# Kernel optimization log

Measured on AMD Instinct MI355X. Metric: run time of the kernel, lower is better.

The kernel has to match this reference:

```python
import jax, jax.numpy as jnp
from jax import lax
import numpy as np
import math

EMBED_DIM = 1024
NUM_HEADS = 16
REDUCTION = 2


def setup_inputs() -> dict:
    key = jax.random.key(0)
    ks = jax.random.split(key, 11)
    B, N, C = 2, 4096, EMBED_DIM
    s = 1.0 / math.sqrt(C)
    return {
        "x": jax.random.normal(ks[0], (B, N, C), jnp.float32),
        "q_w": jax.random.normal(ks[1], (C, C), jnp.float32) * s,
        "q_b": jax.random.normal(ks[2], (C,), jnp.float32) * s,
        "k_w": jax.random.normal(ks[3], (C, C), jnp.float32) * s,
        "k_b": jax.random.normal(ks[4], (C,), jnp.float32) * s,
        "v_w": jax.random.normal(ks[5], (C, C), jnp.float32) * s,
        "v_b": jax.random.normal(ks[6], (C,), jnp.float32) * s,
        "conv_w": jax.random.normal(ks[7], (C, 1, 3), jnp.float32) * 0.5,
        "conv_b": jax.random.normal(ks[8], (C,), jnp.float32) * 0.1,
        "out_w": jax.random.normal(ks[9], (C, C), jnp.float32) * s,
        "out_b": jax.random.normal(ks[10], (C,), jnp.float32) * s,
    }


def reference(x, q_w, q_b, k_w, k_b, v_w, v_b, conv_w, conv_b, out_w, out_b):
    B, N, C = x.shape
    H = NUM_HEADS
    D = C // H
    scale = 1.0 / math.sqrt(D)

    q = x @ q_w.T + q_b  # [B,N,C]

    # depthwise conv1d KV downsample: kernel=3, stride=REDUCTION, pad=1, groups=C
    xd = jnp.transpose(x, (0, 2, 1))  # [B,C,N]
    xd = lax.conv_general_dilated(
        xd, conv_w, window_strides=(REDUCTION,), padding=[(1, 1)],
        feature_group_count=C, dimension_numbers=("NCH", "OIH", "NCH"))
    xd = xd + conv_b[None, :, None]
    xd = jnp.transpose(xd, (0, 2, 1))  # [B,Nk,C]

    k = xd @ k_w.T + k_b
    v = xd @ v_w.T + v_b

    Nk = k.shape[1]
    q = q.reshape(B, N, H, D).transpose(0, 2, 1, 3)   # [B,H,N,D]
    k = k.reshape(B, Nk, H, D).transpose(0, 2, 1, 3)  # [B,H,Nk,D]
    v = v.reshape(B, Nk, H, D).transpose(0, 2, 1, 3)

    att = jnp.einsum("bhnd,bhmd->bhnm", q, k) * scale  # [B,H,N,Nk]
    att = jax.nn.softmax(att, axis=-1)
    out = jnp.einsum("bhnm,bhmd->bhnd", att, v)        # [B,H,N,D]
    out = out.transpose(0, 2, 1, 3).reshape(B, N, C)
    return out @ out_w.T + out_b
```

## Files before the change

kernel.cpp:

```cpp
#include <hip/hip_runtime.h>
#include <stdint.h>
#include <stddef.h>


using bf16x8 = __attribute__((ext_vector_type(8))) short;
using f32x4  = __attribute__((ext_vector_type(4))) float;
using f32x16 = __attribute__((ext_vector_type(16))) float;
using u16x4  = __attribute__((ext_vector_type(4))) unsigned short;
using u32x4  = __attribute__((ext_vector_type(4))) uint32_t;

#if defined(__has_builtin)
#if __has_builtin(__builtin_amdgcn_exp2f)
#define FAST_EXP2(x) __builtin_amdgcn_exp2f(x)
#endif
#endif
#ifndef FAST_EXP2
extern "C" __device__ float __ocml_native_exp2_f32(float);
#define FAST_EXP2(x) __ocml_native_exp2_f32(x)
#endif

__device__ __forceinline__ unsigned short f2bf(float f) {
  union { float f; uint32_t u; } v; v.f = f;
  uint32_t r = v.u + 0x7fffu + ((v.u >> 16) & 1u);
  return (unsigned short)(r >> 16);
}

__device__ __forceinline__ uint32_t cvt_pk_bf16(float lo, float hi) {
  uint32_t r;
  asm("v_cvt_pk_bf16_f32 %0, %1, %2" : "=v"(r) : "v"(lo), "v"(hi));
  return r;
}

__device__ __forceinline__ void plane32_swap(uint32_t& a, uint32_t& b) {
  asm("v_permlane32_swap_b32 %0, %1" : "+v"(a), "+v"(b));
}

__global__ __launch_bounds__(256)
void cast_bf16_kernel(const float* __restrict__ in, unsigned short* __restrict__ out, int n) {
  int i = (blockIdx.x * 256 + threadIdx.x) * 8;
  if (i >= n) return;
  float4 a = *(const float4*)(in + i);
  float4 b = *(const float4*)(in + i + 4);
  u16x4 r0 = {f2bf(a.x), f2bf(a.y), f2bf(a.z), f2bf(a.w)};
  u16x4 r1 = {f2bf(b.x), f2bf(b.y), f2bf(b.z), f2bf(b.w)};
  *(u16x4*)(out + i) = r0;
  *(u16x4*)(out + i + 4) = r1;
}

struct WPtrs { const float* p0; const float* p1; const float* p2; const float* p3; };
__global__ __launch_bounds__(256)
void cast4_bf16_kernel(WPtrs in, unsigned short* __restrict__ out) {
  int which = blockIdx.x >> 9;
  int i = ((blockIdx.x & 511) * 256 + threadIdx.x) * 8;
  const float* src = (which == 0) ? in.p0 : (which == 1) ? in.p1
                   : (which == 2) ? in.p2 : in.p3;
  unsigned short* dst = out + (size_t)which * 1048576;
  float4 a = *(const float4*)(src + i);
  float4 b = *(const float4*)(src + i + 4);
  u16x4 r0 = {f2bf(a.x), f2bf(a.y), f2bf(a.z), f2bf(a.w)};
  u16x4 r1 = {f2bf(b.x), f2bf(b.y), f2bf(b.z), f2bf(b.w)};
  *(u16x4*)(dst + i) = r0;
  *(u16x4*)(dst + i + 4) = r1;
}

__global__ __launch_bounds__(256)
void conv_ds_kernel(const float* __restrict__ x, const float* __restrict__ cw,
                    const float* __restrict__ cb, unsigned short* __restrict__ xd) {
  int row = blockIdx.x;
  int b = row >> 11, m = row & 2047;
  int c = threadIdx.x * 4;
  const float* xb = x + (size_t)b * 4096 * 1024;
  int n0 = 2 * m - 1;
  float4 x0 = {0.f, 0.f, 0.f, 0.f};
  if (n0 >= 0) x0 = *(const float4*)(xb + (size_t)n0 * 1024 + c);
  float4 x1 = *(const float4*)(xb + (size_t)(2 * m) * 1024 + c);
  float4 x2 = *(const float4*)(xb + (size_t)(2 * m + 1) * 1024 + c);
  float4 w0 = *(const float4*)(cw + c * 3);
  float4 w1 = *(const float4*)(cw + c * 3 + 4);
  float4 w2 = *(const float4*)(cw + c * 3 + 8);
  float4 bb = *(const float4*)(cb + c);
  float r0 = x0.x * w0.x + x1.x * w0.y + x2.x * w0.z + bb.x;
  float r1 = x0.y * w0.w + x1.y * w1.x + x2.y * w1.y + bb.y;
  float r2 = x0.z * w1.z + x1.z * w1.w + x2.z * w2.x + bb.z;
  float r3 = x0.w * w2.y + x1.w * w2.z + x2.w * w2.w + bb.w;
  u16x4 r = {f2bf(r0), f2bf(r1), f2bf(r2), f2bf(r3)};
  *(u16x4*)(xd + (size_t)row * 1024 + c) = r;
}

template<int OUT_MODE>
__global__ __launch_bounds__(256)
void gemm_bt(const unsigned short* __restrict__ A, const unsigned short* __restrict__ W,
             const float* __restrict__ bias, const float* __restrict__ bias2,
             void* __restrict__ out, void* __restrict__ out2,
             int M, int N, int K) {
  __shared__ unsigned short As[128 * 32];
  __shared__ unsigned short Bs[128 * 32];
  const int tid = threadIdx.x;
  const int w = tid >> 6, lane = tid & 63;
  const int nbn = N >> 7;
  const int bm = blockIdx.x / nbn, bn = blockIdx.x % nbn;
  const int wr = w >> 1, wc = w & 1;
  const int l15 = lane & 15, l4 = lane >> 4;

  f32x4 acc[4][4];
#pragma unroll
  for (int m = 0; m < 4; ++m)
#pragma unroll
    for (int n = 0; n < 4; ++n) acc[m][n] = (f32x4)0.0f;

  const int arow = bm * 128 + w * 16 + (lane >> 2);
  const int brow = bn * 128 + w * 16 + (lane >> 2);
  const int kcol = (lane & 3) * 8;

  for (int kt = 0; kt < K; kt += 32) {
#pragma unroll
    for (int p = 0; p < 2; ++p) {
      __builtin_amdgcn_global_load_lds(
          (const __attribute__((address_space(1))) void*)(A + (size_t)(arow + p * 64) * K + kt + kcol),
          (__attribute__((address_space(3))) void*)(As + p * 2048 + w * 512), 16, 0, 0);
      __builtin_amdgcn_global_load_lds(
          (const __attribute__((address_space(1))) void*)(W + (size_t)(brow + p * 64) * K + kt + kcol),
          (__attribute__((address_space(3))) void*)(Bs + p * 2048 + w * 512), 16, 0, 0);
    }
    __syncthreads();
    bf16x8 af[4], bf[4];
#pragma unroll
    for (int m = 0; m < 4; ++m) af[m] = *(const bf16x8*)(As + (wr * 64 + m * 16 + l15) * 32 + l4 * 8);
#pragma unroll
    for (int n = 0; n < 4; ++n) bf[n] = *(const bf16x8*)(Bs + (wc * 64 + n * 16 + l15) * 32 + l4 * 8);
#pragma unroll
    for (int m = 0; m < 4; ++m)
#pragma unroll
      for (int n = 0; n < 4; ++n)
        acc[m][n] = __builtin_amdgcn_mfma_f32_16x16x32_bf16(af[m], bf[n], acc[m][n], 0, 0, 0);
    __syncthreads();
  }

  const bool vregion = (OUT_MODE == 3) && (bn >= 8);
#pragma unroll
  for (int n = 0; n < 4; ++n) {
    int col = bn * 128 + wc * 64 + n * 16 + l15;
    float bv = vregion ? bias2[col - 1024] : bias[col];
#pragma unroll
    for (int m = 0; m < 4; ++m) {
      int row0 = bm * 128 + wr * 64 + m * 16 + l4 * 4;
      if (vregion) {
        int b = row0 >> 11, kv = row0 & 2047;
        u16x4 r = {f2bf(acc[m][n][0] + bv), f2bf(acc[m][n][1] + bv),
                   f2bf(acc[m][n][2] + bv), f2bf(acc[m][n][3] + bv)};
        *(u16x4*)((unsigned short*)out2 + ((size_t)(b * 1024 + (col - 1024))) * 2048 + kv) = r;
      } else if (OUT_MODE == 1 || OUT_MODE == 3) {
        const int ldn = (OUT_MODE == 3) ? 1024 : N;
#pragma unroll
        for (int i = 0; i < 4; ++i)
          ((unsigned short*)out)[(size_t)(row0 + i) * ldn + col] = f2bf(acc[m][n][i] + bv);
      } else {
#pragma unroll
        for (int i = 0; i < 4; ++i)
          ((float*)out)[(size_t)(row0 + i) * N + col] = acc[m][n][i] + bv;
      }
    }
  }
}

#define ATT_SCL_L2E 0.18033688011112043f

__global__ __launch_bounds__(256)
void flash_attn_kernel(const unsigned short* __restrict__ q,
                       const unsigned short* __restrict__ k,
                       const unsigned short* __restrict__ vt,
                       unsigned short* __restrict__ o) {
  const int bid = blockIdx.x;
  const int lin = (bid & 7) * 128 + (bid >> 3);
  const int qb = lin & 31;
  const int hb = lin >> 5;
  const int h = hb & 15, b = hb >> 4;

  const int tid = threadIdx.x;
  const int w = tid >> 6, lane = tid & 63;
  const int l31 = lane & 31, hi = lane >> 5;

  __shared__ unsigned short Ks[2][64 * 64];
  __shared__ unsigned short Vs[2][64 * 64];

  const size_t C = 1024;
  const int qrow = b * 4096 + qb * 128 + w * 32 + l31;

  bf16x8 qf[4];
#pragma unroll
  for (int ks = 0; ks < 4; ++ks)
    qf[ks] = *(const bf16x8*)(q + (size_t)qrow * C + h * 64 + ks * 16 + hi * 8);

  f32x16 o0 = (f32x16)0.0f, o1 = (f32x16)0.0f;
  float lrun = 0.f;

  const int srow = (tid & 7) | ((tid >> 5) << 3);
  const int sc2  = (tid >> 3) & 3;
  const int sxor = (srow & 7);
  const unsigned short* kbase = k  + ((size_t)(b * 2048 + srow)) * C + h * 64;
  const unsigned short* vbase = vt + ((size_t)(b * 1024 + h * 64 + srow)) * 2048;

  const int r0 = l31, r1 = 32 + l31;
  const int x0c = (r0 & 7) * 8, x1c = (r1 & 7) * 8;

  auto exppack = [&](f32x16& s0, f32x16& s1, u32x4 (&pw)[4]) {
    float rs0 = 0.f, rs1 = 0.f;
#pragma unroll
    for (int i = 0; i < 16; ++i) {
      float p0 = FAST_EXP2(s0[i] * ATT_SCL_L2E);
      float p1 = FAST_EXP2(s1[i] * ATT_SCL_L2E);
      s0[i] = p0; s1[i] = p1;
      rs0 += p0; rs1 += p1;
    }
    lrun += rs0 + rs1;
#pragma unroll
    for (int hh = 0; hh < 2; ++hh) {
#pragma unroll
      for (int cp = 0; cp < 2; ++cp) {
#pragma unroll
        for (int e = 0; e < 2; ++e) {
          float xa0 = (hh == 0) ? s0[8 * cp + 2 * e]     : s1[8 * cp + 2 * e];
          float xa1 = (hh == 0) ? s0[8 * cp + 2 * e + 1] : s1[8 * cp + 2 * e + 1];
          float xb0 = (hh == 0) ? s0[8 * cp + 4 + 2 * e]     : s1[8 * cp + 4 + 2 * e];
          float xb1 = (hh == 0) ? s0[8 * cp + 4 + 2 * e + 1] : s1[8 * cp + 4 + 2 * e + 1];
          uint32_t wa = cvt_pk_bf16(xa0, xa1);
          uint32_t wb = cvt_pk_bf16(xb0, xb1);
          plane32_swap(wa, wb);
          pw[2 * hh + cp][e]     = wa;
          pw[2 * hh + cp][e + 2] = wb;
        }
      }
    }
  };

  bf16x8 krg[2], vrg[2], tmp[2];
#pragma unroll
  for (int j = 0; j < 2; ++j) tmp[j] = *(const bf16x8*)(kbase + (sc2 + 4 * j) * 8);
#pragma unroll
  for (int j = 0; j < 2; ++j)
    *(bf16x8*)(&Ks[0][srow * 64 + (((sc2 + 4 * j) ^ sxor) * 8)]) = tmp[j];
#pragma unroll
  for (int j = 0; j < 2; ++j) tmp[j] = *(const bf16x8*)(kbase + (size_t)64 * C + (sc2 + 4 * j) * 8);
#pragma unroll
  for (int j = 0; j < 2; ++j)
    *(bf16x8*)(&Ks[1][srow * 64 + (((sc2 + 4 * j) ^ sxor) * 8)]) = tmp[j];
#pragma unroll
  for (int j = 0; j < 2; ++j) tmp[j] = *(const bf16x8*)(vbase + (sc2 + 4 * j) * 8);
#pragma unroll
  for (int j = 0; j < 2; ++j)
    *(bf16x8*)(&Vs[0][srow * 64 + (((sc2 + 4 * j) ^ sxor) * 8)]) = tmp[j];
#pragma unroll
  for (int j = 0; j < 2; ++j) {
    krg[j] = *(const bf16x8*)(kbase + (size_t)128 * C + (sc2 + 4 * j) * 8);
    vrg[j] = *(const bf16x8*)(vbase + 64 + (sc2 + 4 * j) * 8);
  }
  __syncthreads();

  u32x4 pwA[4], pwB[4];
  {
    f32x16 s0 = (f32x16)0.0f, s1 = (f32x16)0.0f;
    __builtin_amdgcn_s_setprio(1);
#pragma unroll
    for (int ks = 0; ks < 4; ++ks) {
      int coff = ks * 16 + hi * 8;
      bf16x8 kf0 = *(const bf16x8*)(&Ks[0][r0 * 64 + (coff ^ x0c)]);
      bf16x8 kf1 = *(const bf16x8*)(&Ks[0][r1 * 64 + (coff ^ x1c)]);
      s0 = __builtin_amdgcn_mfma_f32_32x32x16_bf16(kf0, qf[ks], s0, 0, 0, 0);
      s1 = __builtin_amdgcn_mfma_f32_32x32x16_bf16(kf1, qf[ks], s1, 0, 0, 0);
    }
    __builtin_amdgcn_s_setprio(0);
    exppack(s0, s1, pwA);
  }
  __syncthreads();

  auto body = [&](int t, u32x4 (&pwC)[4], u32x4 (&pwN)[4]) {
    const unsigned short* Vc = Vs[t & 1];
    f32x16 s0 = (f32x16)0.0f, s1 = (f32x16)0.0f;

    __builtin_amdgcn_s_setprio(1);
    if (t < 31) {
      const unsigned short* Kn = Ks[(t + 1) & 1];
#pragma unroll
      for (int ks = 0; ks < 4; ++ks) {
        int coff = ks * 16 + hi * 8;
        bf16x8 kf0 = *(const bf16x8*)(Kn + r0 * 64 + (coff ^ x0c));
        bf16x8 kf1 = *(const bf16x8*)(Kn + r1 * 64 + (coff ^ x1c));
        s0 = __builtin_amdgcn_mfma_f32_32x32x16_bf16(kf0, qf[ks], s0, 0, 0, 0);
        s1 = __builtin_amdgcn_mfma_f32_32x32x16_bf16(kf1, qf[ks], s1, 0, 0, 0);
      }
    }
#pragma unroll
    for (int ksv = 0; ksv < 4; ++ksv) {
      bf16x8 pv = __builtin_bit_cast(bf16x8, pwC[ksv]);
      int coff = ksv * 16 + hi * 8;
      bf16x8 vf0 = *(const bf16x8*)(Vc + r0 * 64 + (coff ^ x0c));
      bf16x8 vf1 = *(const bf16x8*)(Vc + r1 * 64 + (coff ^ x1c));
      o0 = __builtin_amdgcn_mfma_f32_32x32x16_bf16(vf0, pv, o0, 0, 0, 0);
      o1 = __builtin_amdgcn_mfma_f32_32x32x16_bf16(vf1, pv, o1, 0, 0, 0);
    }
    __builtin_amdgcn_s_setprio(0);

    if (t < 30) {
#pragma unroll
      for (int j = 0; j < 2; ++j)
        *(bf16x8*)(&((unsigned short*)Ks[t & 1])[srow * 64 + (((sc2 + 4 * j) ^ sxor) * 8)]) = krg[j];
    }
    if (t < 31) {
#pragma unroll
      for (int j = 0; j < 2; ++j)
        *(bf16x8*)(&((unsigned short*)Vs[(t + 1) & 1])[srow * 64 + (((sc2 + 4 * j) ^ sxor) * 8)]) = vrg[j];
    }
    if (t < 29) {
#pragma unroll
      for (int j = 0; j < 2; ++j)
        krg[j] = *(const bf16x8*)(kbase + (size_t)(t + 3) * 64 * C + (sc2 + 4 * j) * 8);
    }
    if (t < 30) {
#pragma unroll
      for (int j = 0; j < 2; ++j)
        vrg[j] = *(const bf16x8*)(vbase + (t + 2) * 64 + (sc2 + 4 * j) * 8);
    }

    if (t < 31) exppack(s0, s1, pwN);

    if (t < 31) __syncthreads();
  };

  for (int tt = 0; tt < 16; ++tt) {
    body(2 * tt,     pwA, pwB);
    body(2 * tt + 1, pwB, pwA);
  }

  float lsum = lrun + __shfl_xor(lrun, 32);
  const float inv = 1.0f / lsum;
  u32x4 ow[4];
#pragma unroll
  for (int c = 0; c < 4; ++c) {
#pragma unroll
    for (int e = 0; e < 2; ++e) {
      uint32_t wa = cvt_pk_bf16(o0[4 * c + 2 * e] * inv, o0[4 * c + 2 * e + 1] * inv);
      uint32_t wb = cvt_pk_bf16(o1[4 * c + 2 * e] * inv, o1[4 * c + 2 * e + 1] * inv);
      plane32_swap(wa, wb);
      ow[c][e]     = wa;
      ow[c][e + 2] = wb;
    }
  }
  unsigned short* op = o + (size_t)qrow * C + h * 64 + hi * 32;
#pragma unroll
  for (int ch = 0; ch < 4; ++ch)
    *(u32x4*)(op + ch * 8) = ow[ch];
}

extern "C" void kernel_launch(void* const* d_in, const int* in_sizes, int n_in,
                              void* d_out, int out_size, void* d_ws, size_t ws_size,
                              hipStream_t stream) {
  const float* x   = (const float*)d_in[0];
  const float* q_w = (const float*)d_in[1];
  const float* q_b = (const float*)d_in[2];
  const float* k_w = (const float*)d_in[3];
  const float* k_b = (const float*)d_in[4];
  const float* v_w = (const float*)d_in[5];
  const float* v_b = (const float*)d_in[6];
  const float* cw  = (const float*)d_in[7];
  const float* cb  = (const float*)d_in[8];
  const float* o_w = (const float*)d_in[9];
  const float* o_b = (const float*)d_in[10];
  float* out = (float*)d_out;

  unsigned short* ws    = (unsigned short*)d_ws;
  unsigned short* x_bf  = ws;
  unsigned short* qw_bf = x_bf + 8388608;
  unsigned short* kw_bf = qw_bf + 1048576;
  unsigned short* vw_bf = kw_bf + 1048576;
  unsigned short* ow_bf = vw_bf + 1048576;
  unsigned short* q_bf  = ow_bf + 1048576;
  unsigned short* xd_bf = q_bf + 8388608;
  unsigned short* k_bf  = xd_bf + 4194304;
  unsigned short* vt_bf = k_bf + 4194304;
  unsigned short* ao_bf = x_bf;

  cast_bf16_kernel<<<4096, 256, 0, stream>>>(x, x_bf, 8388608);
  WPtrs wp = {q_w, k_w, v_w, o_w};
  cast4_bf16_kernel<<<2048, 256, 0, stream>>>(wp, qw_bf);
  conv_ds_kernel<<<4096, 256, 0, stream>>>(x, cw, cb, xd_bf);

  gemm_bt<1><<<512, 256, 0, stream>>>(x_bf, qw_bf, q_b, nullptr, q_bf, nullptr,
                                      8192, 1024, 1024);
  gemm_bt<3><<<512, 256, 0, stream>>>(xd_bf, kw_bf, k_b, v_b, k_bf, vt_bf,
                                      4096, 2048, 1024);

  flash_attn_kernel<<<1024, 256, 0, stream>>>(q_bf, k_bf, vt_bf, ao_bf);

  gemm_bt<0><<<512, 256, 0, stream>>>(ao_bf, ow_bf, o_b, nullptr, out, nullptr,
                                      8192, 1024, 1024);
}
```

Measured before the change: 208.3 us.

## Fuse x cast into conv kernel, prescale Q, swizzle GEMM block order

Folds the fp32-to-bf16 cast of x into the depthwise conv kernel, which already loads rows 2m and 2m+1, so x is read from HBM only once and one launch goes away. The softmax scale times log2(e) is applied in the Q projection epilogue, which removes a multiply per score in the attention exp loop. GEMM block indices are also remapped in a stride-8 swizzle to change the tile scheduling order. Rounding Q to bf16 after scaling slightly changes its numerics.

```diff
diff --git a/kernel.cpp b/kernel.cpp
--- a/kernel.cpp
+++ b/kernel.cpp
@@ -8,6 +8,8 @@
 using f32x16 = __attribute__((ext_vector_type(16))) float;
 using u16x4  = __attribute__((ext_vector_type(4))) unsigned short;
 using u32x4  = __attribute__((ext_vector_type(4))) uint32_t;
+
+#define ATT_SCL_L2E 0.18033688011112043f
 
 #if defined(__has_builtin)
 #if __has_builtin(__builtin_amdgcn_exp2f)
@@ -33,18 +35,6 @@
 
 __device__ __forceinline__ void plane32_swap(uint32_t& a, uint32_t& b) {
   asm("v_permlane32_swap_b32 %0, %1" : "+v"(a), "+v"(b));
-}
-
-__global__ __launch_bounds__(256)
-void cast_bf16_kernel(const float* __restrict__ in, unsigned short* __restrict__ out, int n) {
-  int i = (blockIdx.x * 256 + threadIdx.x) * 8;
-  if (i >= n) return;
-  float4 a = *(const float4*)(in + i);
-  float4 b = *(const float4*)(in + i + 4);
-  u16x4 r0 = {f2bf(a.x), f2bf(a.y), f2bf(a.z), f2bf(a.w)};
-  u16x4 r1 = {f2bf(b.x), f2bf(b.y), f2bf(b.z), f2bf(b.w)};
-  *(u16x4*)(out + i) = r0;
-  *(u16x4*)(out + i + 4) = r1;
 }
 
 struct WPtrs { const float* p0; const float* p1; const float* p2; const float* p3; };
@@ -64,8 +54,9 @@
 }
 
 __global__ __launch_bounds__(256)
-void conv_ds_kernel(const float* __restrict__ x, const float* __restrict__ cw,
-                    const float* __restrict__ cb, unsigned short* __restrict__ xd) {
+void conv_cast_kernel(const float* __restrict__ x, const float* __restrict__ cw,
+                      const float* __restrict__ cb, unsigned short* __restrict__ xd,
+                      unsigned short* __restrict__ x_bf) {
   int row = blockIdx.x;
   int b = row >> 11, m = row & 2047;
   int c = threadIdx.x * 4;
@@ -85,6 +76,11 @@
   float r3 = x0.w * w2.y + x1.w * w2.z + x2.w * w2.w + bb.w;
   u16x4 r = {f2bf(r0), f2bf(r1), f2bf(r2), f2bf(r3)};
   *(u16x4*)(xd + (size_t)row * 1024 + c) = r;
+  unsigned short* xbf_b = x_bf + (size_t)b * 4096 * 1024;
+  u16x4 c1 = {f2bf(x1.x), f2bf(x1.y), f2bf(x1.z), f2bf(x1.w)};
+  u16x4 c2 = {f2bf(x2.x), f2bf(x2.y), f2bf(x2.z), f2bf(x2.w)};
+  *(u16x4*)(xbf_b + (size_t)(2 * m) * 1024 + c) = c1;
+  *(u16x4*)(xbf_b + (size_t)(2 * m + 1) * 1024 + c) = c2;
 }
 
 template<int OUT_MODE>
@@ -98,7 +94,8 @@
   const int tid = threadIdx.x;
   const int w = tid >> 6, lane = tid & 63;
   const int nbn = N >> 7;
-  const int bm = blockIdx.x / nbn, bn = blockIdx.x % nbn;
+  const int swz = (blockIdx.x & 7) * 64 + (blockIdx.x >> 3);
+  const int bm = swz / nbn, bn = swz % nbn;
   const int wr = w >> 1, wc = w & 1;
   const int l15 = lane & 15, l4 = lane >> 4;
 
@@ -149,11 +146,15 @@
         u16x4 r = {f2bf(acc[m][n][0] + bv), f2bf(acc[m][n][1] + bv),
                    f2bf(acc[m][n][2] + bv), f2bf(acc[m][n][3] + bv)};
         *(u16x4*)((unsigned short*)out2 + ((size_t)(b * 1024 + (col - 1024))) * 2048 + kv) = r;
-      } else if (OUT_MODE == 1 || OUT_MODE == 3) {
-        const int ldn = (OUT_MODE == 3) ? 1024 : N;
+      } else if (OUT_MODE == 1) {
 #pragma unroll
         for (int i = 0; i < 4; ++i)
-          ((unsigned short*)out)[(size_t)(row0 + i) * ldn + col] = f2bf(acc[m][n][i] + bv);
+          ((unsigned short*)out)[(size_t)(row0 + i) * N + col] =
+              f2bf((acc[m][n][i] + bv) * ATT_SCL_L2E);
+      } else if (OUT_MODE == 3) {
+#pragma unroll
+        for (int i = 0; i < 4; ++i)
+          ((unsigned short*)out)[(size_t)(row0 + i) * 1024 + col] = f2bf(acc[m][n][i] + bv);
       } else {
 #pragma unroll
         for (int i = 0; i < 4; ++i)
@@ -162,8 +163,6 @@
     }
   }
 }
-
-#define ATT_SCL_L2E 0.18033688011112043f
 
 __global__ __launch_bounds__(256)
 void flash_attn_kernel(const unsigned short* __restrict__ q,
@@ -207,8 +206,8 @@
     float rs0 = 0.f, rs1 = 0.f;
 #pragma unroll
     for (int i = 0; i < 16; ++i) {
-      float p0 = FAST_EXP2(s0[i] * ATT_SCL_L2E);
-      float p1 = FAST_EXP2(s1[i] * ATT_SCL_L2E);
+      float p0 = FAST_EXP2(s0[i]);
+      float p1 = FAST_EXP2(s1[i]);
       s0[i] = p0; s1[i] = p1;
       rs0 += p0; rs1 += p1;
     }
@@ -379,10 +378,9 @@
   unsigned short* vt_bf = k_bf + 4194304;
   unsigned short* ao_bf = x_bf;
 
-  cast_bf16_kernel<<<4096, 256, 0, stream>>>(x, x_bf, 8388608);
   WPtrs wp = {q_w, k_w, v_w, o_w};
   cast4_bf16_kernel<<<2048, 256, 0, stream>>>(wp, qw_bf);
-  conv_ds_kernel<<<4096, 256, 0, stream>>>(x, cw, cb, xd_bf);
+  conv_cast_kernel<<<4096, 256, 0, stream>>>(x, cw, cb, xd_bf, x_bf);
 
   gemm_bt<1><<<512, 256, 0, stream>>>(x_bf, qw_bf, q_b, nullptr, q_bf, nullptr,
                                       8192, 1024, 1024);
```

After: 194.2 us. 6.8% less time.
